# Performance work log

Hardware: AMD Instinct MI355X
Metric: run time of the kernel (lower is better)

## Reference

```python
import jax, jax.numpy as jnp
import numpy as np

DIM = 64
H = 4
POS_DIM = 4
NUM_IDS = 16
B = 2048
N = 64


def setup_inputs() -> dict:
    key = jax.random.key(0)
    ks = jax.random.split(key, 16)
    d8 = DIM // 8
    stdv = 1.0 / np.sqrt(DIM * DIM)
    inp = {
        "x": jax.random.normal(ks[0], (B, N, DIM), jnp.float32),
        "pos": jax.random.normal(ks[1], (B, N, POS_DIM), jnp.float32),
        "strength": jax.random.normal(ks[2], (512,), jnp.float32),
        "embed_id1": 3,
        # weights stored [in, out] (torch Linear weight transposed)
        "Wq": jax.random.normal(ks[3], (DIM, DIM), jnp.float32) * 0.05,
        "Wk": jax.random.normal(ks[4], (DIM, DIM), jnp.float32) * 0.05,
        "pos_W1": jax.random.normal(ks[5], (POS_DIM, POS_DIM), jnp.float32) * 0.3,
        "pos_b1": jnp.zeros((POS_DIM,), jnp.float32),
        "pos_W2": jax.random.normal(ks[6], (POS_DIM, d8), jnp.float32) * 0.3,
        "pos_b2": jnp.zeros((d8,), jnp.float32),
        "head_W": jax.random.normal(ks[7], (d8, H), jnp.float32) * 0.3,
        "head_b": jnp.zeros((H,), jnp.float32),
        "gate": jnp.ones((H,), jnp.float32),
        "embeds": jax.random.uniform(ks[8], (NUM_IDS, DIM * DIM), jnp.float32, -stdv, stdv),
        "out_W": jax.random.normal(ks[9], (DIM, DIM), jnp.float32) * 0.05,
        "out_b": jnp.zeros((DIM,), jnp.float32),
        "str_W": jax.random.normal(ks[10], (512, 64), jnp.float32) * 0.04,
        "str_b": jnp.zeros((64,), jnp.float32),
    }
    return inp


def reference(x, pos, strength, embed_id1, Wq, Wk, pos_W1, pos_b1, pos_W2, pos_b2,
              head_W, head_b, gate, embeds, out_W, out_b, str_W, str_b):
    Bb, Nn, dim = x.shape
    h = gate.shape[0]
    dh = dim // h

    # strength projection, added to dynamic-weight V
    s64 = strength @ str_W + str_b                       # [dim]
    E = embeds[embed_id1].reshape(dim, dim)              # per-sample V weight
    v = x @ E.T + s64                                    # F.linear(x, E) + strength
    v = v.reshape(Bb, Nn, h, dh).transpose(0, 2, 1, 3)   # [B,H,N,dh]

    # QK attention
    q = (x @ Wq).reshape(Bb, Nn, h, dh).transpose(0, 2, 1, 3)
    k = (x @ Wk).reshape(Bb, Nn, h, dh).transpose(0, 2, 1, 3)
    attn = jax.nn.softmax(jnp.einsum('bhqd,bhkd->bhqk', q, k) / np.sqrt(dh), axis=-1)

    # pairwise relative-position attention
    p = jax.nn.relu(pos @ pos_W1 + pos_b1) @ pos_W2 + pos_b2          # [B,N,dim//8]
    diff = p[:, :, None, :] - p[:, None, :, :]                        # [B,N,N,dim//8]
    pos_logits = jnp.einsum('bqkf,fh->bhqk', diff, head_W) + head_b[None, :, None, None]
    pos_attn = jax.nn.softmax(pos_logits, axis=-1)

    # sigmoid-gated mixing + renormalization
    g = jax.nn.sigmoid(gate)[None, :, None, None]
    attn = (1.0 - g) * attn + g * pos_attn
    attn = attn / jnp.sum(attn, axis=-1, keepdims=True)

    out = jnp.einsum('bhqk,bhkd->bhqd', attn, v)
    out = out.transpose(0, 2, 1, 3).reshape(Bb, Nn, dim)
    return out @ out_W + out_b
```

## Files before the change

kernel.cpp:

```cpp
#include <hip/hip_runtime.h>

typedef unsigned short u16;
typedef unsigned int u32;
typedef short bf8 __attribute__((ext_vector_type(8)));
typedef float f4v __attribute__((ext_vector_type(4)));
typedef float f16v __attribute__((ext_vector_type(16)));

#define STR 72

__device__ __forceinline__ u32 f2bf(float f){
    union{float f;u32 i;}c; c.f=f; u32 i=c.i;
    return (i + 0x7FFFu + ((i>>16)&1u)) >> 16;
}

__device__ __forceinline__ u32 cvtpk(float lo, float hi){
    u32 r; asm("v_cvt_pk_bf16_f32 %0, %1, %2" : "=v"(r) : "v"(lo), "v"(hi)); return r;
}
__device__ __forceinline__ short cvt1(float v){
    u32 r; asm("v_cvt_pk_bf16_f32 %0, %1, %2" : "=v"(r) : "v"(v), "v"(v)); return (short)r;
}

__device__ __forceinline__ void stage_row16(const float* __restrict__ g, short* __restrict__ dst,
                                            int n, int c0){
    const float4* p = (const float4*)(g + n*64 + c0);
    float4 a=p[0], b=p[1], c=p[2], d=p[3];
    uint4 o0, o1;
    o0.x = cvtpk(a.x,a.y); o0.y = cvtpk(a.z,a.w);
    o0.z = cvtpk(b.x,b.y); o0.w = cvtpk(b.z,b.w);
    o1.x = cvtpk(c.x,c.y); o1.y = cvtpk(c.z,c.w);
    o1.z = cvtpk(d.x,d.y); o1.w = cvtpk(d.z,d.w);
    *(uint4*)&dst[n*STR + c0]     = o0;
    *(uint4*)&dst[n*STR + c0 + 8] = o1;
}

__global__ __launch_bounds__(256) void pre_kernel(
    const int* __restrict__ embed_id,
    const float* __restrict__ Wq, const float* __restrict__ Wk, const float* __restrict__ oW,
    const float* __restrict__ embeds, const float* __restrict__ sW, const float* __restrict__ sb,
    const float* __restrict__ strength,
    float* __restrict__ ws_s64, u16* __restrict__ ws_wq, u16* __restrict__ ws_wk,
    u16* __restrict__ ws_ow, u16* __restrict__ ws_e)
{
    const int j = blockIdx.x;
    const int t = threadIdx.x;

    if (j < 3) {
        const float* W = (j==0) ? Wq : (j==1) ? Wk : oW;
        u16* dst = (j==0) ? ws_wq : (j==1) ? ws_wk : ws_ow;
        const float scl = (j==0) ? 0.25f : 1.0f;
        const int kp = t >> 3, ng = t & 7;
        const float4* r0 = (const float4*)(W + (2*kp  )*64 + 8*ng);
        const float4* r1 = (const float4*)(W + (2*kp+1)*64 + 8*ng);
        float4 a0=r0[0], a1=r0[1], b0=r1[0], b1=r1[1];
        float lo[8]={a0.x,a0.y,a0.z,a0.w,a1.x,a1.y,a1.z,a1.w};
        float hi[8]={b0.x,b0.y,b0.z,b0.w,b1.x,b1.y,b1.z,b1.w};
        #pragma unroll
        for (int i=0;i<8;++i)
            *(u32*)&dst[(8*ng+i)*64 + 2*kp] = f2bf(scl*lo[i]) | (f2bf(scl*hi[i])<<16);
    } else {
        __shared__ float sp[4][64];
        {
            const int n = t >> 2, c0 = (t & 3) << 4;
            const float4* p = (const float4*)(embeds + (size_t)(*embed_id)*4096 + n*64 + c0);
            float4 a=p[0], b=p[1], c=p[2], d=p[3];
            uint4 o0, o1;
            o0.x = f2bf(a.x)|(f2bf(a.y)<<16); o0.y = f2bf(a.z)|(f2bf(a.w)<<16);
            o0.z = f2bf(b.x)|(f2bf(b.y)<<16); o0.w = f2bf(b.z)|(f2bf(b.w)<<16);
            o1.x = f2bf(c.x)|(f2bf(c.y)<<16); o1.y = f2bf(c.z)|(f2bf(c.w)<<16);
            o1.z = f2bf(d.x)|(f2bf(d.y)<<16); o1.w = f2bf(d.z)|(f2bf(d.w)<<16);
            *(uint4*)&ws_e[n*64 + c0]     = o0;
            *(uint4*)&ws_e[n*64 + c0 + 8] = o1;
        }
        {
            const int d = t & 63, part = t >> 6;
            const float* wp = sW + part*128*64 + d;
            const float* s  = strength + part*128;
            float acc = 0.f;
            #pragma unroll 8
            for (int i = 0; i < 128; ++i) acc = fmaf(s[i], wp[i*64], acc);
            sp[part][d] = acc;
        }
        __syncthreads();
        if (t < 64) ws_s64[t] = sp[0][t] + sp[1][t] + sp[2][t] + sp[3][t] + sb[t];
    }
}

__global__ __launch_bounds__(256, 3) void attn_main_kernel(
    const float* __restrict__ x, const float* __restrict__ pos,
    const float* __restrict__ gate, const float* __restrict__ ob,
    const float* __restrict__ pW1, const float* __restrict__ pb1,
    const float* __restrict__ pW2, const float* __restrict__ pb2,
    const float* __restrict__ hW,
    const float* __restrict__ ws_s64,
    const u16* __restrict__ ws_wq, const u16* __restrict__ ws_wk,
    const u16* __restrict__ ws_ow, const u16* __restrict__ ws_e,
    float* __restrict__ out)
{
    __shared__ short B0[64*STR];
    __shared__ short PX[64*STR];
    __shared__ short B2[64*STR];
    __shared__ short B3[64*STR];
    __shared__ short VT[64*STR];

    const int t    = threadIdx.x;
    const int b    = blockIdx.x;
    const int lane = t & 63;
    const int w    = t >> 6;
    const int l15  = lane & 15;
    const int l31  = lane & 31;
    const int l5   = lane >> 5;
    const int quad = lane >> 4;
    const int n    = t >> 2;
    const int c0   = (t & 3) << 4;

    const int wq_off = (16*w + l15)*64 + quad*8;
    bf8 bq0 = *(const bf8*)&ws_wq[wq_off];
    bf8 bq1 = *(const bf8*)&ws_wq[wq_off + 32];
    bf8 bk0 = *(const bf8*)&ws_wk[wq_off];
    bf8 bk1 = *(const bf8*)&ws_wk[wq_off + 32];
    bf8 be0 = *(const bf8*)&ws_e [wq_off];
    bf8 be1 = *(const bf8*)&ws_e [wq_off + 32];
    bf8 bo0 = *(const bf8*)&ws_ow[wq_off];
    bf8 bo1 = *(const bf8*)&ws_ow[wq_off + 32];
    const float sv  = ws_s64[16*w + l15];
    const float obv = ob[16*w + l15];
    const float g   = 1.f/(1.f + __expf(-gate[w]));

    stage_row16(x + (size_t)b*4096, B0, n, c0);

    float patk;
    {
        const float4 pv = *(const float4*)(pos + ((size_t)b*64 + lane)*4);
        float h1[4], p8[8];
        #pragma unroll
        for (int jj = 0; jj < 4; ++jj){
            float a = pb1[jj];
            a = fmaf(pv.x, pW1[0*4+jj], a);
            a = fmaf(pv.y, pW1[1*4+jj], a);
            a = fmaf(pv.z, pW1[2*4+jj], a);
            a = fmaf(pv.w, pW1[3*4+jj], a);
            h1[jj] = fmaxf(a, 0.f);
        }
        #pragma unroll
        for (int f = 0; f < 8; ++f){
            float a = pb2[f];
            #pragma unroll
            for (int jj = 0; jj < 4; ++jj) a = fmaf(h1[jj], pW2[jj*8+f], a);
            p8[f] = a;
        }
        float tv = 0.f;
        #pragma unroll
        for (int f = 0; f < 8; ++f) tv = fmaf(p8[f], hW[f*4+w], tv);
        float e = __expf(-tv);
        float ssum = e;
        #pragma unroll
        for (int off = 32; off; off >>= 1) ssum += __shfl_xor(ssum, off);
        patk = g * (e / ssum);
    }
    __syncthreads();

    float pg = 0.f;
    #pragma unroll
    for (int mt=0; mt<4; ++mt){
        bf8 a0 = *(const bf8*)&B0[(16*mt + l15)*STR + quad*8];
        bf8 a1 = *(const bf8*)&B0[(16*mt + l15)*STR + 32 + quad*8];
        f4v cq, ck, cv;
        #pragma unroll
        for (int r=0;r<4;++r){ cq[r]=0.f; ck[r]=0.f; cv[r]=sv; }
        __builtin_amdgcn_s_setprio(1);
        cq = __builtin_amdgcn_mfma_f32_16x16x32_bf16(a0, bq0, cq, 0,0,0);
        cq = __builtin_amdgcn_mfma_f32_16x16x32_bf16(a1, bq1, cq, 0,0,0);
        ck = __builtin_amdgcn_mfma_f32_16x16x32_bf16(a0, bk0, ck, 0,0,0);
        ck = __builtin_amdgcn_mfma_f32_16x16x32_bf16(a1, bk1, ck, 0,0,0);
        cv = __builtin_amdgcn_mfma_f32_16x16x32_bf16(a0, be0, cv, 0,0,0);
        cv = __builtin_amdgcn_mfma_f32_16x16x32_bf16(a1, be1, cv, 0,0,0);
        __builtin_amdgcn_s_setprio(0);
        #pragma unroll
        for (int r=0;r<4;++r){
            B2[(16*mt + 4*quad + r)*STR + 16*w + l15] = cvt1(cq[r]);
            B3[(16*mt + 4*quad + r)*STR + 16*w + l15] = cvt1(ck[r]);
            pg = fmaf(__shfl(patk, 16*mt + 4*quad + r), cv[r], pg);
        }
        uint2 pk;
        pk.x = cvtpk(cv[0], cv[1]);
        pk.y = cvtpk(cv[2], cv[3]);
        *(uint2*)&VT[(16*w + l15)*STR + 16*mt + 4*quad] = pk;
    }
    pg += __shfl_xor(pg, 16);
    pg += __shfl_xor(pg, 32);
    asm volatile("" ::: "memory");

    f16v S[2][2];
    {
        bf8 ka0 = *(const bf8*)&B3[(     l31)*STR + 16*w + 8*l5];
        bf8 ka1 = *(const bf8*)&B3[(32 + l31)*STR + 16*w + 8*l5];
        bf8 qb0 = *(const bf8*)&B2[(     l31)*STR + 16*w + 8*l5];
        bf8 qb1 = *(const bf8*)&B2[(32 + l31)*STR + 16*w + 8*l5];
        #pragma unroll
        for (int mt=0;mt<2;++mt)
            #pragma unroll
            for (int nt=0;nt<2;++nt)
                #pragma unroll
                for (int i=0;i<16;++i) S[mt][nt][i] = 0.f;
        __builtin_amdgcn_s_setprio(1);
        S[0][0] = __builtin_amdgcn_mfma_f32_32x32x16_bf16(ka0, qb0, S[0][0], 0,0,0);
        S[0][1] = __builtin_amdgcn_mfma_f32_32x32x16_bf16(ka0, qb1, S[0][1], 0,0,0);
        S[1][0] = __builtin_amdgcn_mfma_f32_32x32x16_bf16(ka1, qb0, S[1][0], 0,0,0);
        S[1][1] = __builtin_amdgcn_mfma_f32_32x32x16_bf16(ka1, qb1, S[1][1], 0,0,0);
        __builtin_amdgcn_s_setprio(0);
    }
    float c1_[2];
    #pragma unroll
    for (int nt=0;nt<2;++nt){
        float p[16];
        #pragma unroll
        for (int i=0;i<16;++i){
            float a  = __expf(S[0][nt][i]); S[0][nt][i] = a;
            float bb = __expf(S[1][nt][i]); S[1][nt][i] = bb;
            p[i] = a + bb;
        }
        #pragma unroll
        for (int s=8; s; s>>=1)
            #pragma unroll
            for (int i=0;i<s;++i) p[i] += p[i+s];
        float l = p[0] + __shfl_xor(p[0], 32);
        c1_[nt] = (1.f - g) / l;
    }
    __syncthreads();

    short* Pb = (w==0) ? B0 : (w==1) ? PX : (w==2) ? B2 : B3;
    #pragma unroll
    for (int nt=0;nt<2;++nt)
        #pragma unroll
        for (int mt=0;mt<2;++mt)
            #pragma unroll
            for (int rg=0;rg<4;++rg){
                float v0 = S[mt][nt][rg*4+0]*c1_[nt], v1 = S[mt][nt][rg*4+1]*c1_[nt];
                float v2 = S[mt][nt][rg*4+2]*c1_[nt], v3 = S[mt][nt][rg*4+3]*c1_[nt];
                uint2 pk;
                pk.x = cvtpk(v0, v1);
                pk.y = cvtpk(v2, v3);
                *(uint2*)&Pb[(32*nt + l31)*STR + 32*mt + 8*rg + 4*l5] = pk;
            }
    asm volatile("" ::: "memory");

    f4v o[4];
    {
        bf8 bv0 = *(const bf8*)&VT[(16*w + l15)*STR + quad*8];
        bf8 bv1 = *(const bf8*)&VT[(16*w + l15)*STR + 32 + quad*8];
        #pragma unroll
        for (int mt=0;mt<4;++mt){
            o[mt][0]=0.f;o[mt][1]=0.f;o[mt][2]=0.f;o[mt][3]=0.f;
            bf8 a0 = *(const bf8*)&Pb[(16*mt + l15)*STR + quad*8];
            bf8 a1 = *(const bf8*)&Pb[(16*mt + l15)*STR + 32 + quad*8];
            __builtin_amdgcn_s_setprio(1);
            o[mt] = __builtin_amdgcn_mfma_f32_16x16x32_bf16(a0, bv0, o[mt], 0,0,0);
            o[mt] = __builtin_amdgcn_mfma_f32_16x16x32_bf16(a1, bv1, o[mt], 0,0,0);
            __builtin_amdgcn_s_setprio(0);
        }
    }
    __syncthreads();

    #pragma unroll
    for (int mt=0;mt<4;++mt)
        #pragma unroll
        for (int r=0;r<4;++r)
            B3[(16*mt + 4*quad + r)*STR + 16*w + l15] = cvt1(o[mt][r] + pg);
    __syncthreads();

    #pragma unroll
    for (int mt=0;mt<4;++mt){
        bf8 ca0 = *(const bf8*)&B3[(16*mt + l15)*STR + quad*8];
        bf8 ca1 = *(const bf8*)&B3[(16*mt + l15)*STR + 32 + quad*8];
        f4v c;
        #pragma unroll
        for (int r=0;r<4;++r) c[r] = obv;
        __builtin_amdgcn_s_setprio(1);
        c = __builtin_amdgcn_mfma_f32_16x16x32_bf16(ca0, bo0, c, 0,0,0);
        c = __builtin_amdgcn_mfma_f32_16x16x32_bf16(ca1, bo1, c, 0,0,0);
        __builtin_amdgcn_s_setprio(0);
        #pragma unroll
        for (int r=0;r<4;++r)
            out[((size_t)b*64 + 16*mt + quad*4 + r)*64 + 16*w + l15] = c[r];
    }
}

extern "C" void kernel_launch(void* const* d_in, const int* in_sizes, int n_in,
                              void* d_out, int out_size, void* d_ws, size_t ws_size,
                              hipStream_t stream) {
    const int B = in_sizes[0] / (64 * 64);

    float* ws_s64 = (float*)d_ws;
    u16*   ws_wq  = (u16*)(ws_s64 + 64);
    u16*   ws_wk  = ws_wq + 4096;
    u16*   ws_ow  = ws_wk + 4096;
    u16*   ws_e   = ws_ow + 4096;

    pre_kernel<<<4, 256, 0, stream>>>(
        (const int*)d_in[3],
        (const float*)d_in[4],  (const float*)d_in[5],  (const float*)d_in[14],
        (const float*)d_in[13], (const float*)d_in[16], (const float*)d_in[17],
        (const float*)d_in[2],
        ws_s64, ws_wq, ws_wk, ws_ow, ws_e);

    attn_main_kernel<<<B, 256, 0, stream>>>(
        (const float*)d_in[0],  (const float*)d_in[1],
        (const float*)d_in[12], (const float*)d_in[15],
        (const float*)d_in[6],  (const float*)d_in[7],  (const float*)d_in[8],  (const float*)d_in[9],
        (const float*)d_in[10],
        ws_s64, ws_wq, ws_wk, ws_ow, ws_e,
        (float*)d_out);
}
```

Before: 131.7 us.

## Keep attention probabilities in registers, feed PV MFMA via lane shuffles

The softmax scores are no longer written to a per-wave LDS buffer and read back for the P·V product. They are repacked in registers with cross-half-wave shuffles into 32x32x16 MFMA operands, and the result goes straight to B3 with the pg bias added. This removes one LDS buffer, two block barriers and an LDS round trip per score tile. In exchange it adds shuffle and select instructions and raises register pressure, and the write into B3 while other waves may still be reading K from B3 deserves scrutiny.

```diff
diff --git a/kernel.cpp b/kernel.cpp
--- a/kernel.cpp
+++ b/kernel.cpp
@@ -97,7 +97,6 @@
     float* __restrict__ out)
 {
     __shared__ short B0[64*STR];
-    __shared__ short PX[64*STR];
     __shared__ short B2[64*STR];
     __shared__ short B3[64*STR];
     __shared__ short VT[64*STR];
@@ -190,33 +189,32 @@
     pg += __shfl_xor(pg, 32);
     asm volatile("" ::: "memory");
 
-    f16v S[2][2];
-    {
-        bf8 ka0 = *(const bf8*)&B3[(     l31)*STR + 16*w + 8*l5];
-        bf8 ka1 = *(const bf8*)&B3[(32 + l31)*STR + 16*w + 8*l5];
-        bf8 qb0 = *(const bf8*)&B2[(     l31)*STR + 16*w + 8*l5];
-        bf8 qb1 = *(const bf8*)&B2[(32 + l31)*STR + 16*w + 8*l5];
-        #pragma unroll
-        for (int mt=0;mt<2;++mt)
-            #pragma unroll
-            for (int nt=0;nt<2;++nt)
-                #pragma unroll
-                for (int i=0;i<16;++i) S[mt][nt][i] = 0.f;
+    bf8 ka0 = *(const bf8*)&B3[(     l31)*STR + 16*w + 8*l5];
+    bf8 ka1 = *(const bf8*)&B3[(32 + l31)*STR + 16*w + 8*l5];
+    const int vrow = (16*w + l15)*STR + 8*l5;
+    bf8 av0 = *(const bf8*)&VT[vrow];
+    bf8 av1 = *(const bf8*)&VT[vrow + 16];
+    bf8 av2 = *(const bf8*)&VT[vrow + 32];
+    bf8 av3 = *(const bf8*)&VT[vrow + 48];
+    float pgd[8];
+    #pragma unroll
+    for (int j=0;j<8;++j) pgd[j] = __shfl(pg, 8*(j>>2) + 4*l5 + (j&3));
+
+    #pragma unroll
+    for (int nt=0; nt<2; ++nt){
+        bf8 qb = *(const bf8*)&B2[(32*nt + l31)*STR + 16*w + 8*l5];
+        f16v S0, S1, O;
+        #pragma unroll
+        for (int i=0;i<16;++i){ S0[i]=0.f; S1[i]=0.f; O[i]=0.f; }
         __builtin_amdgcn_s_setprio(1);
-        S[0][0] = __builtin_amdgcn_mfma_f32_32x32x16_bf16(ka0, qb0, S[0][0], 0,0,0);
-        S[0][1] = __builtin_amdgcn_mfma_f32_32x32x16_bf16(ka0, qb1, S[0][1], 0,0,0);
-        S[1][0] = __builtin_amdgcn_mfma_f32_32x32x16_bf16(ka1, qb0, S[1][0], 0,0,0);
-        S[1][1] = __builtin_amdgcn_mfma_f32_32x32x16_bf16(ka1, qb1, S[1][1], 0,0,0);
+        S0 = __builtin_amdgcn_mfma_f32_32x32x16_bf16(ka0, qb, S0, 0,0,0);
+        S1 = __builtin_amdgcn_mfma_f32_32x32x16_bf16(ka1, qb, S1, 0,0,0);
         __builtin_amdgcn_s_setprio(0);
-    }
-    float c1_[2];
-    #pragma unroll
-    for (int nt=0;nt<2;++nt){
         float p[16];
         #pragma unroll
         for (int i=0;i<16;++i){
-            float a  = __expf(S[0][nt][i]); S[0][nt][i] = a;
-            float bb = __expf(S[1][nt][i]); S[1][nt][i] = bb;
+            float a  = __expf(S0[i]); S0[i] = a;
+            float bb = __expf(S1[i]); S1[i] = bb;
             p[i] = a + bb;
         }
         #pragma unroll
@@ -224,48 +222,36 @@
             #pragma unroll
             for (int i=0;i<s;++i) p[i] += p[i+s];
         float l = p[0] + __shfl_xor(p[0], 32);
-        c1_[nt] = (1.f - g) / l;
-    }
-    __syncthreads();
-
-    short* Pb = (w==0) ? B0 : (w==1) ? PX : (w==2) ? B2 : B3;
-    #pragma unroll
-    for (int nt=0;nt<2;++nt)
-        #pragma unroll
-        for (int mt=0;mt<2;++mt)
-            #pragma unroll
-            for (int rg=0;rg<4;++rg){
-                float v0 = S[mt][nt][rg*4+0]*c1_[nt], v1 = S[mt][nt][rg*4+1]*c1_[nt];
-                float v2 = S[mt][nt][rg*4+2]*c1_[nt], v3 = S[mt][nt][rg*4+3]*c1_[nt];
-                uint2 pk;
-                pk.x = cvtpk(v0, v1);
-                pk.y = cvtpk(v2, v3);
-                *(uint2*)&Pb[(32*nt + l31)*STR + 32*mt + 8*rg + 4*l5] = pk;
-            }
-    asm volatile("" ::: "memory");
-
-    f4v o[4];
-    {
-        bf8 bv0 = *(const bf8*)&VT[(16*w + l15)*STR + quad*8];
-        bf8 bv1 = *(const bf8*)&VT[(16*w + l15)*STR + 32 + quad*8];
-        #pragma unroll
-        for (int mt=0;mt<4;++mt){
-            o[mt][0]=0.f;o[mt][1]=0.f;o[mt][2]=0.f;o[mt][3]=0.f;
-            bf8 a0 = *(const bf8*)&Pb[(16*mt + l15)*STR + quad*8];
-            bf8 a1 = *(const bf8*)&Pb[(16*mt + l15)*STR + 32 + quad*8];
-            __builtin_amdgcn_s_setprio(1);
-            o[mt] = __builtin_amdgcn_mfma_f32_16x16x32_bf16(a0, bv0, o[mt], 0,0,0);
-            o[mt] = __builtin_amdgcn_mfma_f32_16x16x32_bf16(a1, bv1, o[mt], 0,0,0);
-            __builtin_amdgcn_s_setprio(0);
-        }
-    }
-    __syncthreads();
-
-    #pragma unroll
-    for (int mt=0;mt<4;++mt)
-        #pragma unroll
-        for (int r=0;r<4;++r)
-            B3[(16*mt + 4*quad + r)*STR + 16*w + l15] = cvt1(o[mt][r] + pg);
+        float c1s = (1.f - g) / l;
+
+        #define PV_STEP(Sm, k0, av)                                              \
+        {                                                                        \
+            u32 a_lo = cvtpk(c1s*Sm[k0+0], c1s*Sm[k0+1]);                        \
+            u32 a_hi = cvtpk(c1s*Sm[k0+2], c1s*Sm[k0+3]);                        \
+            u32 b_lo = cvtpk(c1s*Sm[k0+4], c1s*Sm[k0+5]);                        \
+            u32 b_hi = cvtpk(c1s*Sm[k0+6], c1s*Sm[k0+7]);                        \
+            u32 sl = l5 ? a_lo : b_lo, sh = l5 ? a_hi : b_hi;                    \
+            u32 rl = (u32)__shfl_xor((int)sl, 32);                               \
+            u32 rh = (u32)__shfl_xor((int)sh, 32);                               \
+            union { u32 u[4]; bf8 v; } F;                                        \
+            F.u[0] = l5 ? rl : a_lo; F.u[1] = l5 ? rh : a_hi;                    \
+            F.u[2] = l5 ? b_lo : rl; F.u[3] = l5 ? b_hi : rh;                    \
+            O = __builtin_amdgcn_mfma_f32_32x32x16_bf16(av, F.v, O, 0,0,0);      \
+        }
+        PV_STEP(S0, 0, av0)
+        PV_STEP(S0, 8, av1)
+        PV_STEP(S1, 0, av2)
+        PV_STEP(S1, 8, av3)
+        #undef PV_STEP
+
+        #pragma unroll
+        for (int rg=0; rg<2; ++rg){
+            uint2 pk;
+            pk.x = cvtpk(O[4*rg+0]+pgd[4*rg+0], O[4*rg+1]+pgd[4*rg+1]);
+            pk.y = cvtpk(O[4*rg+2]+pgd[4*rg+2], O[4*rg+3]+pgd[4*rg+3]);
+            *(uint2*)&B3[(32*nt + l31)*STR + 16*w + 8*rg + 4*l5] = pk;
+        }
+    }
     __syncthreads();
 
     #pragma unroll
```

Result: no change. 133.6 us (+1.4%).
